# Kernel optimization log

Measured on AMD Instinct MI355X. Metric: run time of the kernel, lower is better.

Reference implementation:

```python
import jax, jax.numpy as jnp
import numpy as np

N_NODES = 10000
N_EDGES = 160000
R_CUT = 1.4415
N_RBF = 20


def silu(x):
    return x * jax.nn.sigmoid(x)


def setup_inputs() -> dict:
    key = jax.random.key(0)
    ks = jax.random.split(key, 12)
    x = jax.random.normal(ks[0], (N_NODES, 512), jnp.float32)
    edge_index = jax.random.randint(ks[1], (2, N_EDGES), 0, N_NODES, dtype=jnp.int64)
    ea1 = jax.random.normal(ks[2], (N_EDGES, 3), jnp.float32)
    edge_attr1 = ea1 / jnp.linalg.norm(ea1, axis=1, keepdims=True)  # unit edge vectors
    # edge lengths in (0.1, 1.4) so bessel 1/r is well-conditioned and inside r_cut
    edge_attr2 = jax.random.uniform(ks[3], (N_EDGES,), jnp.float32) * 1.3 + 0.1

    def lin(k, fi, fo):
        return (jax.random.normal(k, (fi, fo), jnp.float32) / np.sqrt(fi)).astype(jnp.float32)

    return {
        "x": x, "edge_index": edge_index,
        "edge_attr1": edge_attr1, "edge_attr2": edge_attr2,
        # PAINNMessage params (stored [in,out]; y = x @ W + b)
        "W1": lin(ks[4], 128, 128), "b1": jnp.zeros(128, jnp.float32),
        "W2": lin(ks[5], 20, 384), "b2": jnp.zeros(384, jnp.float32),
        "W3": lin(ks[6], 128, 384), "b3": jnp.zeros(384, jnp.float32),
        # PAINNUpdate params
        "U": lin(ks[7], 128, 128), "V": lin(ks[8], 128, 128),
        "Wu1": lin(ks[9], 256, 128), "bu1": jnp.zeros(128, jnp.float32),
        "Wu2": lin(ks[10], 128, 384), "bu2": jnp.zeros(384, jnp.float32),
    }


def _painn_block(x, edge_index, edge_attr1, edge_attr2,
                 W1, b1, W2, b2, W3, b3, U, V, Wu1, bu1, Wu2, bu2):
    src, dst = edge_index[0], edge_index[1]
    E = src.shape[0]

    # ---------- PAINNMessage ----------
    x_j = x[src]                                   # gather [E,512]
    v_j = x_j[:, :384].reshape(E, 128, 3)          # vector channels
    s_j = x_j[:, 384:]                             # scalar channels [E,128]
    s_j = silu(s_j @ W1 + b1) @ W3 + b3            # [E,384]

    r = edge_attr2[:, None]                        # [E,1]
    n = jnp.arange(1, N_RBF + 1, dtype=x.dtype)    # [20]
    rbf = jnp.sqrt(2.0 / R_CUT) * jnp.sin(n * jnp.pi * r / R_CUT) / r  # [E,20]
    cutoff = 0.5 * (jnp.cos(jnp.pi * r / R_CUT) + 1.0) * (r < R_CUT)
    edge_basis = (rbf * cutoff) @ W2 + b2          # [E,384]

    split = s_j * edge_basis
    s1, s2, s3 = split[:, :128], split[:, 128:256], split[:, 256:]
    # v_j * split_1 + outer(split_3, unit_edge_vec)
    v_msg = v_j * s1[:, :, None] + s3[:, :, None] * edge_attr1[:, None, :]  # [E,128,3]
    msg = jnp.concatenate([v_msg.reshape(E, 384), s2], axis=1)              # [E,512]
    x = x + jax.ops.segment_sum(msg, dst, num_segments=N_NODES)

    # ---------- PAINNUpdate ----------
    x_j = x[src]                                   # [E,512]
    v = x_j[:, :384].reshape(E, 3, 128)            # (torch .view semantics)
    v = v @ U                                      # [E,3,128]
    v_V = v @ V                                    # [E,3,128]
    v = v.reshape(E, 128, 3)                       # plain reshape, as in torch .view
    v_V = v_V.reshape(E, 128, 3)
    norm = jnp.linalg.norm(v_V, axis=2)            # [E,128]
    s = x_j[:, 384:]
    h = silu(jnp.concatenate([norm, s], axis=1) @ Wu1 + bu1) @ Wu2 + bu2  # [E,384]
    s1, s2, s3 = h[:, :128], h[:, 128:256], h[:, 256:]  # s2 is unused in original
    v = v * s1[:, :, None]
    dot = jnp.einsum('ijk,ijk->ij', v, v_V)        # [E,128]
    scal = dot + s3                                # [E,128]
    msg = jnp.concatenate([v.reshape(E, 384), scal], axis=1)  # [E,512]
    x = x + jax.ops.segment_sum(msg, dst, num_segments=N_NODES)
    return x


def reference(x, edge_index, edge_attr1, edge_attr2,
              W1, b1, W2, b2, W3, b3, U, V, Wu1, bu1, Wu2, bu2):
    return _painn_block(x, edge_index, edge_attr1, edge_attr2,
                        W1, b1, W2, b2, W3, b3, U, V, Wu1, bu1, Wu2, bu2)
```

## Files before the change

kernel.cpp:

```cpp
#include <hip/hip_runtime.h>
#include <hip/hip_bf16.h>

#define N_NODES 10000
#define N_EDGES 160000
#define FEAT 512
#define D 128
#define NRBF 20
#define RCUT 1.4415f
#define CAP 64

typedef __attribute__((ext_vector_type(8))) short bf16x8;
typedef __attribute__((ext_vector_type(4))) float f32x4;

__device__ __forceinline__ float silu_f(float x) { return x / (1.0f + __expf(-x)); }
__device__ __forceinline__ float s2f(short s) {
    unsigned int u = ((unsigned int)(unsigned short)s) << 16;
    float f; __builtin_memcpy(&f, &u, 4); return f;
}
__device__ __forceinline__ short f2s(float f) {
    __hip_bfloat16 h = __float2bfloat16(f);
    short s; __builtin_memcpy(&s, &h, 2); return s;
}
__device__ __forceinline__ float asf(unsigned int u) {
    float f; __builtin_memcpy(&f, &u, 4); return f;
}

__global__ __launch_bounds__(256) void k_fill_basis(
    const int* __restrict__ ei, const float* __restrict__ ea2,
    int* __restrict__ cnt, unsigned int* __restrict__ slot,
    __hip_bfloat16* __restrict__ basis)
{
    int e = blockIdx.x * 256 + threadIdx.x;
    if (e >= N_EDGES) return;
    int d = ei[N_EDGES + e];
    int pos = atomicAdd(&cnt[d], 1);
    if (pos < CAP)
        slot[d * CAP + pos] = (((unsigned int)e) << 14) | (unsigned int)ei[e];

    float r  = ea2[e];
    float pr = 3.14159265358979f * r / RCUT;
    float cosv = __cosf(pr);
    float cut  = 0.5f * (cosv + 1.0f) * (r < RCUT ? 1.0f : 0.0f);
    float pref = sqrtf(2.0f / RCUT) / r * cut;
    float c2 = 2.0f * cosv;
    float sm1 = 0.0f, s = __sinf(pr);
    #pragma unroll
    for (int n = 0; n < NRBF; ++n) {
        basis[(size_t)e * NRBF + n] = __float2bfloat16(pref * s);
        float nx = c2 * s - sm1; sm1 = s; s = nx;
    }
}

__global__ __launch_bounds__(256) void k_pack_all(
    const float* __restrict__ W1, const float* __restrict__ W3,
    const float* __restrict__ U,  const float* __restrict__ V,
    const float* __restrict__ Wu1, const float* __restrict__ Wu2,
    short* __restrict__ W1p, short* __restrict__ W3p,
    short* __restrict__ Up,  short* __restrict__ Vp,
    short* __restrict__ Wu1p, short* __restrict__ Wu2p)
{
    int b = blockIdx.x;
    const float* W; short* Wp; int K, N;
    if      (b < 8)  { W = W1;  Wp = W1p;  K = 128; N = 128; }
    else if (b < 32) { W = W3;  Wp = W3p;  K = 128; N = 384; b -= 8;  }
    else if (b < 40) { W = U;   Wp = Up;   K = 128; N = 128; b -= 32; }
    else if (b < 48) { W = V;   Wp = Vp;   K = 128; N = 128; b -= 40; }
    else if (b < 64) { W = Wu1; Wp = Wu1p; K = 256; N = 128; b -= 48; }
    else             { W = Wu2; Wp = Wu2p; K = 128; N = 384; b -= 64; }
    int idx = b * 256 + threadIdx.x;
    int NT = N >> 4;
    int total = (K >> 5) * NT * 64;
    if (idx >= total) return;
    int lane = idx & 63, fid = idx >> 6;
    int ks = fid / NT, ct = fid % NT;
    int k0 = ks * 32 + ((lane >> 4) << 3);
    int c  = ct * 16 + (lane & 15);
    short* o = Wp + (size_t)idx * 8;
    #pragma unroll
    for (int j = 0; j < 8; ++j)
        o[j] = f2s(W[(size_t)(k0 + j) * N + c]);
}

#define LDSP 136
__global__ __launch_bounds__(256) void k_A_mfma(
    const float* __restrict__ x,
    const short* __restrict__ W1p, const float* __restrict__ b1,
    const short* __restrict__ W3p, const float* __restrict__ b3,
    __hip_bfloat16* __restrict__ P1)
{
    __shared__ __align__(16) short sj[16 * LDSP];
    __shared__ __align__(16) short tt[16 * LDSP];
    const int t = threadIdx.x;
    const int lane = t & 63, wave = t >> 6;
    const int n0 = blockIdx.x * 16;

    for (int i = t; i < 16 * 128; i += 256) {
        int e = i >> 7, j = i & 127;
        sj[e * LDSP + j] = f2s(x[(size_t)(n0 + e) * FEAT + 384 + j]);
    }
    for (int i = t; i < 16 * 384; i += 256) {
        int e = i / 384, o = i % 384;
        int j = o & 127, c = o >> 7;
        P1[(size_t)(n0 + e) * 1024 + j * 8 + 3 + c] =
            __float2bfloat16(x[(size_t)(n0 + e) * FEAT + 3 * j + c]);
    }
    __syncthreads();

    {
        f32x4 acc[2];
        #pragma unroll
        for (int q = 0; q < 2; ++q) acc[q] = (f32x4){0.f, 0.f, 0.f, 0.f};
        for (int ks = 0; ks < 4; ++ks) {
            bf16x8 a = *(const bf16x8*)&sj[(lane & 15) * LDSP + ks * 32 + ((lane >> 4) << 3)];
            #pragma unroll
            for (int q = 0; q < 2; ++q) {
                bf16x8 b = ((const bf16x8*)W1p)[((size_t)ks * 8 + wave * 2 + q) * 64 + lane];
                acc[q] = __builtin_amdgcn_mfma_f32_16x16x32_bf16(a, b, acc[q], 0, 0, 0);
            }
        }
        #pragma unroll
        for (int q = 0; q < 2; ++q) {
            int col = (wave * 2 + q) * 16 + (lane & 15);
            int row = (lane >> 4) << 2;
            float bb = b1[col];
            #pragma unroll
            for (int r = 0; r < 4; ++r)
                tt[(row + r) * LDSP + col] = f2s(silu_f(acc[q][r] + bb));
        }
    }
    __syncthreads();

    {
        f32x4 acc[6];
        #pragma unroll
        for (int q = 0; q < 6; ++q) acc[q] = (f32x4){0.f, 0.f, 0.f, 0.f};
        for (int ks = 0; ks < 4; ++ks) {
            bf16x8 a = *(const bf16x8*)&tt[(lane & 15) * LDSP + ks * 32 + ((lane >> 4) << 3)];
            #pragma unroll
            for (int q = 0; q < 6; ++q) {
                bf16x8 b = ((const bf16x8*)W3p)[((size_t)ks * 24 + wave * 6 + q) * 64 + lane];
                acc[q] = __builtin_amdgcn_mfma_f32_16x16x32_bf16(a, b, acc[q], 0, 0, 0);
            }
        }
        #pragma unroll
        for (int q = 0; q < 6; ++q) {
            int col = (wave * 6 + q) * 16 + (lane & 15);
            int row = (lane >> 4) << 2;
            float bb = b3[col];
            #pragma unroll
            for (int r = 0; r < 4; ++r)
                P1[(size_t)(n0 + row + r) * 1024 + (col & 127) * 8 + (col >> 7)] =
                    __float2bfloat16(acc[q][r] + bb);
        }
    }
}

__global__ __launch_bounds__(256) void k_B_mfma(
    const short* __restrict__ Up, const short* __restrict__ Vp,
    const short* __restrict__ Wu1p, const float* __restrict__ bu1,
    const short* __restrict__ Wu2p, const float* __restrict__ bu2,
    const float* __restrict__ xin,
    __hip_bfloat16* __restrict__ M2)
{
    __shared__ __align__(16) short XV[48 * LDSP];
    __shared__ __align__(16) short VU[48 * LDSP];
    __shared__ __align__(16) short S [16 * LDSP];
    __shared__ __align__(16) short NRM[16 * LDSP];
    __shared__ __align__(16) short H1[16 * LDSP];
    __shared__ __align__(16) short A1[16 * LDSP];
    __shared__ __align__(16) short A3[16 * LDSP];

    const int t = threadIdx.x, lane = t & 63, wave = t >> 6;
    const int n0 = blockIdx.x * 16;

    for (int i = t; i < 16 * 512; i += 256) {
        int e = i >> 9, f = i & 511;
        short sv = f2s(xin[(size_t)(n0 + e) * FEAT + f]);
        if (f < 384) XV[(e * 3 + (f >> 7)) * LDSP + (f & 127)] = sv;
        else         S[e * LDSP + (f - 384)] = sv;
    }
    __syncthreads();

    {
        f32x4 acc[3][2];
        #pragma unroll
        for (int rt = 0; rt < 3; ++rt)
            #pragma unroll
            for (int q = 0; q < 2; ++q) acc[rt][q] = (f32x4){0.f, 0.f, 0.f, 0.f};
        for (int ks = 0; ks < 4; ++ks) {
            bf16x8 b[2];
            #pragma unroll
            for (int q = 0; q < 2; ++q)
                b[q] = ((const bf16x8*)Up)[((size_t)ks * 8 + wave * 2 + q) * 64 + lane];
            #pragma unroll
            for (int rt = 0; rt < 3; ++rt) {
                bf16x8 a = *(const bf16x8*)&XV[(rt * 16 + (lane & 15)) * LDSP + ks * 32 + ((lane >> 4) << 3)];
                #pragma unroll
                for (int q = 0; q < 2; ++q)
                    acc[rt][q] = __builtin_amdgcn_mfma_f32_16x16x32_bf16(a, b[q], acc[rt][q], 0, 0, 0);
            }
        }
        #pragma unroll
        for (int rt = 0; rt < 3; ++rt)
            #pragma unroll
            for (int q = 0; q < 2; ++q) {
                int col = (wave * 2 + q) * 16 + (lane & 15);
                int row = rt * 16 + ((lane >> 4) << 2);
                #pragma unroll
                for (int r = 0; r < 4; ++r)
                    VU[(row + r) * LDSP + col] = f2s(acc[rt][q][r]);
            }
    }
    __syncthreads();

    {
        f32x4 acc[3][2];
        #pragma unroll
        for (int rt = 0; rt < 3; ++rt)
            #pragma unroll
            for (int q = 0; q < 2; ++q) acc[rt][q] = (f32x4){0.f, 0.f, 0.f, 0.f};
        for (int ks = 0; ks < 4; ++ks) {
            bf16x8 b[2];
            #pragma unroll
            for (int q = 0; q < 2; ++q)
                b[q] = ((const bf16x8*)Vp)[((size_t)ks * 8 + wave * 2 + q) * 64 + lane];
            #pragma unroll
            for (int rt = 0; rt < 3; ++rt) {
                bf16x8 a = *(const bf16x8*)&VU[(rt * 16 + (lane & 15)) * LDSP + ks * 32 + ((lane >> 4) << 3)];
                #pragma unroll
                for (int q = 0; q < 2; ++q)
                    acc[rt][q] = __builtin_amdgcn_mfma_f32_16x16x32_bf16(a, b[q], acc[rt][q], 0, 0, 0);
            }
        }
        __syncthreads();
        #pragma unroll
        for (int rt = 0; rt < 3; ++rt)
            #pragma unroll
            for (int q = 0; q < 2; ++q) {
                int col = (wave * 2 + q) * 16 + (lane & 15);
                int row = rt * 16 + ((lane >> 4) << 2);
                #pragma unroll
                for (int r = 0; r < 4; ++r)
                    XV[(row + r) * LDSP + col] = f2s(acc[rt][q][r]);
            }
    }
    __syncthreads();

    for (int i = t; i < 16 * 128; i += 256) {
        int nl = i >> 7, j = i & 127;
        float s = 0.f;
        #pragma unroll
        for (int c = 0; c < 3; ++c) {
            int q = 3 * j + c;
            float f = s2f(XV[(nl * 3 + (q >> 7)) * LDSP + (q & 127)]);
            s += f * f;
        }
        NRM[nl * LDSP + j] = f2s(sqrtf(s));
    }
    __syncthreads();

    {
        f32x4 acc[2];
        #pragma unroll
        for (int q = 0; q < 2; ++q) acc[q] = (f32x4){0.f, 0.f, 0.f, 0.f};
        for (int ks = 0; ks < 8; ++ks) {
            const short* asrc = (ks < 4) ? NRM : S;
            int k0 = (ks & 3) * 32;
            bf16x8 a = *(const bf16x8*)&asrc[(lane & 15) * LDSP + k0 + ((lane >> 4) << 3)];
            #pragma unroll
            for (int q = 0; q < 2; ++q) {
                bf16x8 b = ((const bf16x8*)Wu1p)[((size_t)ks * 8 + wave * 2 + q) * 64 + lane];
                acc[q] = __builtin_amdgcn_mfma_f32_16x16x32_bf16(a, b, acc[q], 0, 0, 0);
            }
        }
        #pragma unroll
        for (int q = 0; q < 2; ++q) {
            int col = (wave * 2 + q) * 16 + (lane & 15);
            int row = (lane >> 4) << 2;
            float bb = bu1[col];
            #pragma unroll
            for (int r = 0; r < 4; ++r)
                H1[(row + r) * LDSP + col] = f2s(silu_f(acc[q][r] + bb));
        }
    }
    __syncthreads();

    {
        f32x4 acc[4];
        #pragma unroll
        for (int q = 0; q < 4; ++q) acc[q] = (f32x4){0.f, 0.f, 0.f, 0.f};
        for (int ks = 0; ks < 4; ++ks) {
            bf16x8 a = *(const bf16x8*)&H1[(lane & 15) * LDSP + ks * 32 + ((lane >> 4) << 3)];
            #pragma unroll
            for (int q = 0; q < 4; ++q) {
                int w = wave * 4 + q;
                int ctp = (w < 8) ? w : (16 + (w - 8));
                bf16x8 b = ((const bf16x8*)Wu2p)[((size_t)ks * 24 + ctp) * 64 + lane];
                acc[q] = __builtin_amdgcn_mfma_f32_16x16x32_bf16(a, b, acc[q], 0, 0, 0);
            }
        }
        #pragma unroll
        for (int q = 0; q < 4; ++q) {
            int w = wave * 4 + q;
            int colloc = (w & 7) * 16 + (lane & 15);
            int row = (lane >> 4) << 2;
            short* dst = (w < 8) ? A1 : A3;
            float bb = bu2[((w < 8) ? 0 : 256) + colloc];
            #pragma unroll
            for (int r = 0; r < 4; ++r)
                dst[(row + r) * LDSP + colloc] = f2s(acc[q][r] + bb);
        }
    }
    __syncthreads();

    for (int i = t; i < 16 * 128; i += 256) {
        int nl = i >> 7, j = i & 127;
        float a1v = s2f(A1[nl * LDSP + j]);
        float a3v = s2f(A3[nl * LDSP + j]);
        __hip_bfloat16* mrow = M2 + (size_t)(n0 + nl) * FEAT;
        float dot = 0.f;
        #pragma unroll
        for (int c = 0; c < 3; ++c) {
            int q = 3 * j + c;
            int rr = nl * 3 + (q >> 7), cc = q & 127;
            float vu_ = s2f(VU[rr * LDSP + cc]);
            float vv_ = s2f(XV[rr * LDSP + cc]);
            float vf = vu_ * a1v;
            dot += vf * vv_;
            mrow[c * 128 + j] = __float2bfloat16(vf);
        }
        mrow[384 + j] = __float2bfloat16(dot + a3v);
    }
}

__global__ __launch_bounds__(128) void k_gather1(
    const float* __restrict__ x,
    const __hip_bfloat16* __restrict__ P1,
    const __hip_bfloat16* __restrict__ basis,
    const float* __restrict__ ea1,
    const float* __restrict__ W2, const float* __restrict__ b2,
    const int* __restrict__ cnt, const unsigned int* __restrict__ slot,
    float* __restrict__ out)
{
    __shared__ float ebl[CAP][NRBF];
    __shared__ float eall[CAP][3];
    __shared__ int srcl[CAP], ell[CAP];

    const int d = blockIdx.x, t = threadIdx.x;

    float w2r0[NRBF], w2r1[NRBF], w2r2[NRBF];
    #pragma unroll
    for (int n = 0; n < NRBF; ++n) {
        w2r0[n] = W2[n * 384 + t];
        w2r1[n] = W2[n * 384 + 128 + t];
        w2r2[n] = W2[n * 384 + 256 + t];
    }
    const float b2a = b2[t], b2b = b2[128 + t], b2c = b2[256 + t];

    const int deg = min(cnt[d], CAP);
    if (t < deg) {
        unsigned int p = slot[d * CAP + t];
        srcl[t] = (int)(p & 16383u);
        ell[t]  = (int)(p >> 14);
    }
    __syncthreads();
    for (int i = t; i < deg * NRBF; i += 128)
        ebl[i / NRBF][i % NRBF] = __bfloat162float(basis[(size_t)ell[i / NRBF] * NRBF + (i % NRBF)]);
    for (int i = t; i < deg * 3; i += 128)
        eall[i / 3][i % 3] = ea1[(size_t)ell[i / 3] * 3 + (i % 3)];
    __syncthreads();

    float acc0 = 0.f, acc1 = 0.f, acc2 = 0.f, accs = 0.f;

    for (int base = 0; base < deg; base += 8) {
        uint4 fr[8];
        #pragma unroll
        for (int ee = 0; ee < 8; ++ee) {
            int idx = (base + ee < deg) ? (base + ee) : base;
            fr[ee] = *(const uint4*)(P1 + (size_t)srcl[idx] * 1024 + t * 8);
        }
        #pragma unroll
        for (int ee = 0; ee < 8; ++ee) {
            if (base + ee >= deg) break;
            const int ix = base + ee;
            float ebA = b2a, ebB = b2b, ebC = b2c;
            #pragma unroll
            for (int n = 0; n < NRBF; ++n) {
                float e = ebl[ix][n];
                ebA += e * w2r0[n];
                ebB += e * w2r1[n];
                ebC += e * w2r2[n];
            }
            uint4 u = fr[ee];
            float a1 = asf(u.x << 16), a2 = asf(u.x & 0xffff0000u);
            float a3 = asf(u.y << 16), x0 = asf(u.y & 0xffff0000u);
            float x1 = asf(u.z << 16), x2 = asf(u.z & 0xffff0000u);
            float s1 = a1 * ebA;
            float s2 = a2 * ebB;
            float s3 = a3 * ebC;
            acc0 += x0 * s1 + s3 * eall[ix][0];
            acc1 += x1 * s1 + s3 * eall[ix][1];
            acc2 += x2 * s1 + s3 * eall[ix][2];
            accs += s2;
        }
    }

    const size_t ro = (size_t)d * FEAT;
    out[ro + 3 * t]     = x[ro + 3 * t]     + acc0;
    out[ro + 3 * t + 1] = x[ro + 3 * t + 1] + acc1;
    out[ro + 3 * t + 2] = x[ro + 3 * t + 2] + acc2;
    out[ro + 384 + t]   = x[ro + 384 + t]   + accs;
}

__global__ __launch_bounds__(256) void k_gather2(
    const __hip_bfloat16* __restrict__ M2,
    const int* __restrict__ cnt, const unsigned int* __restrict__ slot,
    float* __restrict__ out)
{
    __shared__ float row[FEAT];
    __shared__ int sl[CAP];
    const int d = blockIdx.x, t = threadIdx.x;
    const int deg = min(cnt[d], CAP);
    if (t < deg) sl[t] = (int)(slot[d * CAP + t] & 16383u);
    __syncthreads();

    float a0 = 0.0f, a1 = 0.0f;
    int i = 0;
    for (; i + 8 <= deg; i += 8) {
        __hip_bfloat162 v[8];
        #pragma unroll
        for (int q = 0; q < 8; ++q)
            v[q] = ((const __hip_bfloat162*)(M2 + (size_t)sl[i + q] * FEAT))[t];
        #pragma unroll
        for (int q = 0; q < 8; ++q) {
            a0 += __bfloat162float(v[q].x);
            a1 += __bfloat162float(v[q].y);
        }
    }
    for (; i < deg; ++i) {
        __hip_bfloat162 v = ((const __hip_bfloat162*)(M2 + (size_t)sl[i] * FEAT))[t];
        a0 += __bfloat162float(v.x);
        a1 += __bfloat162float(v.y);
    }
    row[2 * t]     = a0;
    row[2 * t + 1] = a1;
    __syncthreads();
    #pragma unroll
    for (int gi = 0; gi < 2; ++gi) {
        int g = t + gi * 256;
        int m = (g < 384) ? ((g % 3) * 128 + g / 3) : g;
        out[(size_t)d * FEAT + g] += row[m];
    }
}

extern "C" void kernel_launch(void* const* d_in, const int* in_sizes, int n_in,
                              void* d_out, int out_size, void* d_ws, size_t ws_size,
                              hipStream_t stream) {
    (void)in_sizes; (void)n_in; (void)out_size; (void)ws_size;
    const float* x   = (const float*)d_in[0];
    const int*   ei  = (const int*)d_in[1];
    const float* ea1 = (const float*)d_in[2];
    const float* ea2 = (const float*)d_in[3];
    const float* W1  = (const float*)d_in[4];
    const float* b1  = (const float*)d_in[5];
    const float* W2  = (const float*)d_in[6];
    const float* b2  = (const float*)d_in[7];
    const float* W3  = (const float*)d_in[8];
    const float* b3  = (const float*)d_in[9];
    const float* U   = (const float*)d_in[10];
    const float* V   = (const float*)d_in[11];
    const float* Wu1 = (const float*)d_in[12];
    const float* bu1 = (const float*)d_in[13];
    const float* Wu2 = (const float*)d_in[14];
    const float* bu2 = (const float*)d_in[15];
    float* out = (float*)d_out;

    char* w = (char*)d_ws;
    __hip_bfloat16* P1    = (__hip_bfloat16*)w;
    __hip_bfloat16* M2    = (__hip_bfloat16*)(w + 20480000);
    __hip_bfloat16* basis = (__hip_bfloat16*)(w + 30720000);
    short* W1p  = (short*)(w + 37120000);
    short* W3p  = (short*)(w + 37152768);
    short* Upk  = (short*)(w + 37251072);
    short* Vpk  = (short*)(w + 37283840);
    short* Wu1p = (short*)(w + 37316608);
    short* Wu2p = (short*)(w + 37382144);
    int*          cnt  = (int*)(w + 37505024);
    unsigned int* slot = (unsigned int*)(w + 37545024);

    hipMemsetAsync(cnt, 0, N_NODES * sizeof(int), stream);
    k_pack_all  <<<88,  256, 0, stream>>>(W1, W3, U, V, Wu1, Wu2,
                                          W1p, W3p, Upk, Vpk, Wu1p, Wu2p);
    k_fill_basis<<<(N_EDGES + 255) / 256, 256, 0, stream>>>(ei, ea2, cnt, slot, basis);

    k_A_mfma    <<<N_NODES / 16, 256, 0, stream>>>(x, W1p, b1, W3p, b3, P1);
    k_gather1   <<<N_NODES,      128, 0, stream>>>(x, P1, basis, ea1, W2, b2, cnt, slot, out);
    k_B_mfma    <<<N_NODES / 16, 256, 0, stream>>>(Upk, Vpk, Wu1p, bu1, Wu2p, bu2, out, M2);
    k_gather2   <<<N_NODES,      256, 0, stream>>>(M2, cnt, slot, out);
}
```

Measured before the change: 250.0 us.

## Merge prep kernels, shrink P1 row padding, restructure gather loads

Merges the weight-pack and basis/slot-fill kernels into one launch to save a kernel launch. Packs P1 rows at 6 bf16 per channel instead of 8, cutting gathered bytes per edge in k_gather1, which now does three 32-bit loads instead of one 128-bit load. Adds an occupancy hint on k_gather1. k_gather2 splits each node's edges across two 128-thread halves with 8-byte loads and combines partial sums in shared memory. The narrower unaligned loads and the extra reduction step may offset part of the bandwidth saving.

```diff
diff --git a/kernel.cpp b/kernel.cpp
--- a/kernel.cpp
+++ b/kernel.cpp
@@ -25,12 +25,41 @@
     float f; __builtin_memcpy(&f, &u, 4); return f;
 }
 
-__global__ __launch_bounds__(256) void k_fill_basis(
+__global__ __launch_bounds__(256) void k_prep(
+    const float* __restrict__ W1, const float* __restrict__ W3,
+    const float* __restrict__ U,  const float* __restrict__ V,
+    const float* __restrict__ Wu1, const float* __restrict__ Wu2,
+    short* __restrict__ W1p, short* __restrict__ W3p,
+    short* __restrict__ Up,  short* __restrict__ Vp,
+    short* __restrict__ Wu1p, short* __restrict__ Wu2p,
     const int* __restrict__ ei, const float* __restrict__ ea2,
     int* __restrict__ cnt, unsigned int* __restrict__ slot,
     __hip_bfloat16* __restrict__ basis)
 {
-    int e = blockIdx.x * 256 + threadIdx.x;
+    int b = blockIdx.x;
+    if (b < 88) {
+        const float* W; short* Wp; int K, N;
+        if      (b < 8)  { W = W1;  Wp = W1p;  K = 128; N = 128; }
+        else if (b < 32) { W = W3;  Wp = W3p;  K = 128; N = 384; b -= 8;  }
+        else if (b < 40) { W = U;   Wp = Up;   K = 128; N = 128; b -= 32; }
+        else if (b < 48) { W = V;   Wp = Vp;   K = 128; N = 128; b -= 40; }
+        else if (b < 64) { W = Wu1; Wp = Wu1p; K = 256; N = 128; b -= 48; }
+        else             { W = Wu2; Wp = Wu2p; K = 128; N = 384; b -= 64; }
+        int idx = b * 256 + threadIdx.x;
+        int NT = N >> 4;
+        int total = (K >> 5) * NT * 64;
+        if (idx >= total) return;
+        int lane = idx & 63, fid = idx >> 6;
+        int ks = fid / NT, ct = fid % NT;
+        int k0 = ks * 32 + ((lane >> 4) << 3);
+        int c  = ct * 16 + (lane & 15);
+        short* o = Wp + (size_t)idx * 8;
+        #pragma unroll
+        for (int j = 0; j < 8; ++j)
+            o[j] = f2s(W[(size_t)(k0 + j) * N + c]);
+        return;
+    }
+    int e = (b - 88) * 256 + threadIdx.x;
     if (e >= N_EDGES) return;
     int d = ei[N_EDGES + e];
     int pos = atomicAdd(&cnt[d], 1);
@@ -49,36 +78,6 @@
         basis[(size_t)e * NRBF + n] = __float2bfloat16(pref * s);
         float nx = c2 * s - sm1; sm1 = s; s = nx;
     }
-}
-
-__global__ __launch_bounds__(256) void k_pack_all(
-    const float* __restrict__ W1, const float* __restrict__ W3,
-    const float* __restrict__ U,  const float* __restrict__ V,
-    const float* __restrict__ Wu1, const float* __restrict__ Wu2,
-    short* __restrict__ W1p, short* __restrict__ W3p,
-    short* __restrict__ Up,  short* __restrict__ Vp,
-    short* __restrict__ Wu1p, short* __restrict__ Wu2p)
-{
-    int b = blockIdx.x;
-    const float* W; short* Wp; int K, N;
-    if      (b < 8)  { W = W1;  Wp = W1p;  K = 128; N = 128; }
-    else if (b < 32) { W = W3;  Wp = W3p;  K = 128; N = 384; b -= 8;  }
-    else if (b < 40) { W = U;   Wp = Up;   K = 128; N = 128; b -= 32; }
-    else if (b < 48) { W = V;   Wp = Vp;   K = 128; N = 128; b -= 40; }
-    else if (b < 64) { W = Wu1; Wp = Wu1p; K = 256; N = 128; b -= 48; }
-    else             { W = Wu2; Wp = Wu2p; K = 128; N = 384; b -= 64; }
-    int idx = b * 256 + threadIdx.x;
-    int NT = N >> 4;
-    int total = (K >> 5) * NT * 64;
-    if (idx >= total) return;
-    int lane = idx & 63, fid = idx >> 6;
-    int ks = fid / NT, ct = fid % NT;
-    int k0 = ks * 32 + ((lane >> 4) << 3);
-    int c  = ct * 16 + (lane & 15);
-    short* o = Wp + (size_t)idx * 8;
-    #pragma unroll
-    for (int j = 0; j < 8; ++j)
-        o[j] = f2s(W[(size_t)(k0 + j) * N + c]);
 }
 
 #define LDSP 136
@@ -101,7 +100,7 @@
     for (int i = t; i < 16 * 384; i += 256) {
         int e = i / 384, o = i % 384;
         int j = o & 127, c = o >> 7;
-        P1[(size_t)(n0 + e) * 1024 + j * 8 + 3 + c] =
+        P1[(size_t)(n0 + e) * 768 + j * 6 + 3 + c] =
             __float2bfloat16(x[(size_t)(n0 + e) * FEAT + 3 * j + c]);
     }
     __syncthreads();
@@ -149,7 +148,7 @@
             float bb = b3[col];
             #pragma unroll
             for (int r = 0; r < 4; ++r)
-                P1[(size_t)(n0 + row + r) * 1024 + (col & 127) * 8 + (col >> 7)] =
+                P1[(size_t)(n0 + row + r) * 768 + (col & 127) * 6 + (col >> 7)] =
                     __float2bfloat16(acc[q][r] + bb);
         }
     }
@@ -333,7 +332,7 @@
     }
 }
 
-__global__ __launch_bounds__(128) void k_gather1(
+__global__ __launch_bounds__(128, 4) void k_gather1(
     const float* __restrict__ x,
     const __hip_bfloat16* __restrict__ P1,
     const __hip_bfloat16* __restrict__ basis,
@@ -373,11 +372,13 @@
     float acc0 = 0.f, acc1 = 0.f, acc2 = 0.f, accs = 0.f;
 
     for (int base = 0; base < deg; base += 8) {
-        uint4 fr[8];
+        unsigned int f0[8], f1[8], f2[8];
         #pragma unroll
         for (int ee = 0; ee < 8; ++ee) {
             int idx = (base + ee < deg) ? (base + ee) : base;
-            fr[ee] = *(const uint4*)(P1 + (size_t)srcl[idx] * 1024 + t * 8);
+            const unsigned int* rp =
+                (const unsigned int*)((const char*)P1 + (size_t)srcl[idx] * 1536) + t * 3;
+            f0[ee] = rp[0]; f1[ee] = rp[1]; f2[ee] = rp[2];
         }
         #pragma unroll
         for (int ee = 0; ee < 8; ++ee) {
@@ -391,10 +392,9 @@
                 ebB += e * w2r1[n];
                 ebC += e * w2r2[n];
             }
-            uint4 u = fr[ee];
-            float a1 = asf(u.x << 16), a2 = asf(u.x & 0xffff0000u);
-            float a3 = asf(u.y << 16), x0 = asf(u.y & 0xffff0000u);
-            float x1 = asf(u.z << 16), x2 = asf(u.z & 0xffff0000u);
+            float a1 = asf(f0[ee] << 16), a2 = asf(f0[ee] & 0xffff0000u);
+            float a3 = asf(f1[ee] << 16), x0 = asf(f1[ee] & 0xffff0000u);
+            float x1 = asf(f2[ee] << 16), x2 = asf(f2[ee] & 0xffff0000u);
             float s1 = a1 * ebA;
             float s2 = a2 * ebB;
             float s3 = a3 * ebC;
@@ -417,39 +417,43 @@
     const int* __restrict__ cnt, const unsigned int* __restrict__ slot,
     float* __restrict__ out)
 {
-    __shared__ float row[FEAT];
+    __shared__ float part[2][FEAT];
     __shared__ int sl[CAP];
     const int d = blockIdx.x, t = threadIdx.x;
+    const int tt = t & 127, g = t >> 7;
     const int deg = min(cnt[d], CAP);
     if (t < deg) sl[t] = (int)(slot[d * CAP + t] & 16383u);
     __syncthreads();
 
-    float a0 = 0.0f, a1 = 0.0f;
-    int i = 0;
-    for (; i + 8 <= deg; i += 8) {
-        __hip_bfloat162 v[8];
-        #pragma unroll
-        for (int q = 0; q < 8; ++q)
-            v[q] = ((const __hip_bfloat162*)(M2 + (size_t)sl[i + q] * FEAT))[t];
-        #pragma unroll
-        for (int q = 0; q < 8; ++q) {
-            a0 += __bfloat162float(v[q].x);
-            a1 += __bfloat162float(v[q].y);
-        }
-    }
-    for (; i < deg; ++i) {
-        __hip_bfloat162 v = ((const __hip_bfloat162*)(M2 + (size_t)sl[i] * FEAT))[t];
-        a0 += __bfloat162float(v.x);
-        a1 += __bfloat162float(v.y);
-    }
-    row[2 * t]     = a0;
-    row[2 * t + 1] = a1;
-    __syncthreads();
+    float a0 = 0.f, a1 = 0.f, a2 = 0.f, a3 = 0.f;
+    int i = g;
+    for (; i + 6 < deg; i += 8) {
+        uint2 v[4];
+        #pragma unroll
+        for (int q = 0; q < 4; ++q)
+            v[q] = *(const uint2*)((const char*)M2 + (size_t)sl[i + 2 * q] * 1024 + tt * 8);
+        #pragma unroll
+        for (int q = 0; q < 4; ++q) {
+            a0 += asf(v[q].x << 16); a1 += asf(v[q].x & 0xffff0000u);
+            a2 += asf(v[q].y << 16); a3 += asf(v[q].y & 0xffff0000u);
+        }
+    }
+    for (; i < deg; i += 2) {
+        uint2 v = *(const uint2*)((const char*)M2 + (size_t)sl[i] * 1024 + tt * 8);
+        a0 += asf(v.x << 16); a1 += asf(v.x & 0xffff0000u);
+        a2 += asf(v.y << 16); a3 += asf(v.y & 0xffff0000u);
+    }
+    part[g][tt * 4]     = a0;
+    part[g][tt * 4 + 1] = a1;
+    part[g][tt * 4 + 2] = a2;
+    part[g][tt * 4 + 3] = a3;
+    __syncthreads();
+
     #pragma unroll
     for (int gi = 0; gi < 2; ++gi) {
-        int g = t + gi * 256;
-        int m = (g < 384) ? ((g % 3) * 128 + g / 3) : g;
-        out[(size_t)d * FEAT + g] += row[m];
+        int gc = t + gi * 256;
+        int m = (gc < 384) ? ((gc % 3) * 128 + gc / 3) : gc;
+        out[(size_t)d * FEAT + gc] += part[0][m] + part[1][m];
     }
 }
 
@@ -477,24 +481,24 @@
 
     char* w = (char*)d_ws;
     __hip_bfloat16* P1    = (__hip_bfloat16*)w;
-    __hip_bfloat16* M2    = (__hip_bfloat16*)(w + 20480000);
-    __hip_bfloat16* basis = (__hip_bfloat16*)(w + 30720000);
-    short* W1p  = (short*)(w + 37120000);
-    short* W3p  = (short*)(w + 37152768);
-    short* Upk  = (short*)(w + 37251072);
-    short* Vpk  = (short*)(w + 37283840);
-    short* Wu1p = (short*)(w + 37316608);
-    short* Wu2p = (short*)(w + 37382144);
-    int*          cnt  = (int*)(w + 37505024);
-    unsigned int* slot = (unsigned int*)(w + 37545024);
+    __hip_bfloat16* M2    = (__hip_bfloat16*)(w + 15360000);
+    __hip_bfloat16* basis = (__hip_bfloat16*)(w + 25600000);
+    short* W1p  = (short*)(w + 32000000);
+    short* W3p  = (short*)(w + 32032768);
+    short* Upk  = (short*)(w + 32131072);
+    short* Vpk  = (short*)(w + 32163840);
+    short* Wu1p = (short*)(w + 32196608);
+    short* Wu2p = (short*)(w + 32262144);
+    int*          cnt  = (int*)(w + 32360448);
+    unsigned int* slot = (unsigned int*)(w + 32400448);
 
     hipMemsetAsync(cnt, 0, N_NODES * sizeof(int), stream);
-    k_pack_all  <<<88,  256, 0, stream>>>(W1, W3, U, V, Wu1, Wu2,
-                                          W1p, W3p, Upk, Vpk, Wu1p, Wu2p);
-    k_fill_basis<<<(N_EDGES + 255) / 256, 256, 0, stream>>>(ei, ea2, cnt, slot, basis);
-
-    k_A_mfma    <<<N_NODES / 16, 256, 0, stream>>>(x, W1p, b1, W3p, b3, P1);
-    k_gather1   <<<N_NODES,      128, 0, stream>>>(x, P1, basis, ea1, W2, b2, cnt, slot, out);
-    k_B_mfma    <<<N_NODES / 16, 256, 0, stream>>>(Upk, Vpk, Wu1p, bu1, Wu2p, bu2, out, M2);
-    k_gather2   <<<N_NODES,      256, 0, stream>>>(M2, cnt, slot, out);
-}
+    k_prep    <<<88 + (N_EDGES + 255) / 256, 256, 0, stream>>>(
+        W1, W3, U, V, Wu1, Wu2, W1p, W3p, Upk, Vpk, Wu1p, Wu2p,
+        ei, ea2, cnt, slot, basis);
+
+    k_A_mfma  <<<N_NODES / 16, 256, 0, stream>>>(x, W1p, b1, W3p, b3, P1);
+    k_gather1 <<<N_NODES,      128, 0, stream>>>(x, P1, basis, ea1, W2, b2, cnt, slot, out);
+    k_B_mfma  <<<N_NODES / 16, 256, 0, stream>>>(Upk, Vpk, Wu1p, bu1, Wu2p, bu2, out, M2);
+    k_gather2 <<<N_NODES,      256, 0, stream>>>(M2, cnt, slot, out);
+}
```

Measured after the change: 238.8 us. 4.5% less time.
